# Kernel tuning notes

Hardware: AMD Instinct MI355X
Metric: run time of the kernel (lower is better)

Reference implementation:

```python
import jax, jax.numpy as jnp
import numpy as np
from jax.scipy.special import logsumexp

EPS = 1e-12  # torch F.normalize eps
SINKHORN_ITERS = 3


def _l2norm(a, axis):
    n = jnp.sqrt(jnp.sum(a * a, axis=axis, keepdims=True))
    return a / jnp.maximum(n, EPS)


def _log_optimal_transport(scores, alpha, iters):
    # scores: [B, m, n]; alpha: scalar dust-bin param
    b, m, n = scores.shape
    bins = jnp.broadcast_to(alpha, (b, 1, n)).astype(scores.dtype)
    Z = jnp.concatenate([scores, bins], axis=1)  # [B, m+1, n]
    norm = -np.log(float(m + n))
    log_mu = jnp.asarray(
        np.concatenate([np.full(m, norm), [np.log(float(n - m)) + norm]]),
        scores.dtype,
    )  # [m+1]
    log_nu = jnp.full((n,), norm, scores.dtype)
    u = jnp.zeros((b, m + 1), scores.dtype)
    v = jnp.zeros((b, n), scores.dtype)
    for _ in range(iters):
        u = log_mu[None, :] - logsumexp(Z + v[:, None, :], axis=2)
        v = log_nu[None, :] - logsumexp(Z + u[:, :, None], axis=1)
    return Z + u[:, :, None] + v[:, None, :] - norm


def _forward(x, t, tw1, tb1, tw2, tb2, cw1, cb1, cw2, cb2, sw1, sb1, sw2, sb2, dust_bin):
    B, C = x.shape[0], x.shape[1]
    xf = x.reshape(B, C, -1)  # [B, C, N], 1x1 convs act per-location
    # cluster features f: [B, l, N]
    h = jax.nn.relu(jnp.einsum('oc,bcn->bon', cw1, xf) + cb1[None, :, None])
    f = jnp.einsum('oc,bcn->bon', cw2, h) + cb2[None, :, None]
    # global token: [B, g]
    tok = jax.nn.relu(t @ tw1.T + tb1) @ tw2.T + tb2
    # assignment scores p: [B, m, N]
    hs = jax.nn.relu(jnp.einsum('oc,bcn->bon', sw1, xf) + sb1[None, :, None])
    p = jnp.einsum('oc,bcn->bon', sw2, hs) + sb2[None, :, None]
    Z = _log_optimal_transport(p, dust_bin, SINKHORN_ITERS)
    P = jnp.exp(Z)[:, :-1, :]  # drop dust bin row -> [B, m, N]
    # VLAD-style aggregation: the repeat/multiply/sum is just a batched matmul
    agg = jnp.einsum('bln,bmn->blm', f, P)  # [B, l, m]
    agg = _l2norm(agg, axis=1).reshape(B, -1)  # intra-normalize over l, flatten l-major
    out = jnp.concatenate([_l2norm(tok, axis=-1), agg], axis=-1)
    return _l2norm(out, axis=-1)


def setup_inputs() -> dict:
    key = jax.random.key(0)
    ks = jax.random.split(key, 14)
    B, C, H, W = 64, 768, 32, 32
    L, M, G, HID = 128, 64, 256, 512

    def p(k, shape):
        return jax.random.normal(k, shape, jnp.float32) * 0.02

    return {
        'x': jax.random.normal(ks[0], (B, C, H, W), jnp.float32),
        't': jax.random.normal(ks[1], (B, C), jnp.float32),
        'tw1': p(ks[2], (HID, C)), 'tb1': jnp.zeros((HID,), jnp.float32),
        'tw2': p(ks[3], (G, HID)), 'tb2': jnp.zeros((G,), jnp.float32),
        'cw1': p(ks[4], (HID, C)), 'cb1': jnp.zeros((HID,), jnp.float32),
        'cw2': p(ks[5], (L, HID)), 'cb2': jnp.zeros((L,), jnp.float32),
        'sw1': p(ks[6], (HID, C)), 'sb1': jnp.zeros((HID,), jnp.float32),
        'sw2': p(ks[7], (M, HID)), 'sb2': jnp.zeros((M,), jnp.float32),
        'dust_bin': jnp.asarray(1.0, jnp.float32),
    }


def reference(x, t, tw1, tb1, tw2, tb2, cw1, cb1, cw2, cb2, sw1, sb1, sw2, sb2, dust_bin):
    return _forward(x, t, tw1, tb1, tw2, tb2, cw1, cb1, cw2, cb2, sw1, sb1, sw2, sb2, dust_bin)
```

## Files before the change

### kernel.cpp

```cpp
#include <hip/hip_runtime.h>
#include <math.h>


#define B_SZ   64
#define C_IN   768
#define N_LOC  1024
#define HID    512
#define L_DIM  128
#define M_DIM  64
#define G_DIM  256
#define OUTD   (G_DIM + L_DIM * M_DIM)

typedef unsigned short u16;
typedef __bf16 bf16x8 __attribute__((ext_vector_type(8)));
typedef float f32x4 __attribute__((ext_vector_type(4)));

typedef const __attribute__((address_space(1))) void* gptr_t;
typedef __attribute__((address_space(3))) void* sptr_t;

__device__ __forceinline__ void load_lds16(const void* g, void* l) {
    __builtin_amdgcn_global_load_lds((gptr_t)g, (sptr_t)l, 16, 0, 0);
}

__device__ __forceinline__ u16 f2bf(float f) {
    unsigned u = __float_as_uint(f);
    u += 0x7fffu + ((u >> 16) & 1u);
    return (u16)(u >> 16);
}
__device__ __forceinline__ float bf2f(u16 h) {
    return __uint_as_float(((unsigned)h) << 16);
}

__device__ __forceinline__ float waveReduceSum(float v) {
#pragma unroll
    for (int off = 32; off > 0; off >>= 1) v += __shfl_xor(v, off, 64);
    return v;
}

__global__ __launch_bounds__(256) void setup_kernel(
        const float* __restrict__ cw1, const float* __restrict__ sw1,
        const float* __restrict__ cw2, const float* __restrict__ sw2,
        u16* __restrict__ cw1p, u16* __restrict__ sw1p,
        u16* __restrict__ cw2p, u16* __restrict__ sw2p,
        const float* __restrict__ t, const float* __restrict__ tw1,
        const float* __restrict__ tb1, float* __restrict__ hidb) {
    __shared__ __align__(16) float tl[C_IN];
    const int blk = blockIdx.x;
    const int tid = threadIdx.x;

    if (blk < 432) {
        const int q = blk * 256 + tid;
        const float* src;
        u16* dst;
        if (q < 98304) {
            int path = q / 49152, r = q % 49152;
            int kch = r / 512, c = r & 511;
            src = (path ? sw1 : cw1) + (size_t)c * C_IN + kch * 8;
            dst = (path ? sw1p : cw1p) + (size_t)r * 8;
        } else {
            int q2 = q - 98304;
            int path = (q2 >= 8192) ? 1 : 0;
            int r = q2 - (path ? 8192 : 0);
            int S2 = path ? M_DIM : L_DIM;
            int k2 = r / (4 * S2), kc = (r / S2) & 3, c = r % S2;
            src = (path ? sw2 : cw2) + (size_t)c * HID + k2 * 32 + kc * 8;
            dst = (path ? sw2p : cw2p) + (size_t)r * 8;
        }
        float4 v0 = *(const float4*)(src);
        float4 v1 = *(const float4*)(src + 4);
        *(ushort4*)(dst) = make_ushort4(f2bf(v0.x), f2bf(v0.y), f2bf(v0.z), f2bf(v0.w));
        *(ushort4*)(dst + 4) = make_ushort4(f2bf(v1.x), f2bf(v1.y), f2bf(v1.z), f2bf(v1.w));
        return;
    }

    const int by = blk - 432;
    const int j0 = (by & 7) * 64;
    const int b = by >> 3;
    const int lane = tid & 63;
    const int wave = tid >> 6;
    for (int i = tid; i < C_IN; i += 256) tl[i] = t[(size_t)b * C_IN + i];
    __syncthreads();
    for (int j = wave; j < 64; j += 4) {
        const int row = j0 + j;
        const float4* wr = (const float4*)(tw1 + (size_t)row * C_IN);
        const float4* tr = (const float4*)tl;
        float s = 0.f;
#pragma unroll
        for (int q = 0; q < 3; ++q) {
            float4 wv = wr[lane + 64 * q];
            float4 tv = tr[lane + 64 * q];
            s += wv.x * tv.x + wv.y * tv.y + wv.z * tv.z + wv.w * tv.w;
        }
        s = waveReduceSum(s);
        if (lane == 0) hidb[(size_t)b * HID + row] = fmaxf(s + tb1[row], 0.f);
    }
}

__global__ __launch_bounds__(256, 2) void fused12(
        const float* __restrict__ x,
        const u16* __restrict__ cw1p, const float* __restrict__ cb1,
        const u16* __restrict__ cw2p, const float* __restrict__ cb2,
        const u16* __restrict__ sw1p, const float* __restrict__ sb1,
        const u16* __restrict__ sw2p, const float* __restrict__ sb2,
        u16* __restrict__ fT, u16* __restrict__ pT) {
    __shared__ __align__(16) u16 LDSu[36864];
    const int tid = threadIdx.x;
    const int lane = tid & 63;
    const int wc = tid >> 6;

    const int id = blockIdx.x + 16 * blockIdx.y + 32 * blockIdx.z;
    const int nid = (id & 7) * 256 + (id >> 3);
    const int bx = nid & 15;
    const int path = (nid >> 4) & 1;
    const int bz = nid >> 5;
    const int r0 = bx * 64;

    const u16* W1p = path ? sw1p : cw1p;
    const float* B1 = path ? sb1 : cb1;
    const u16* W2p = path ? sw2p : cw2p;
    const float* B2 = path ? sb2 : cb2;
    u16* O2 = path ? pT : fT;
    const int S2 = path ? M_DIM : L_DIM;

    const float* xb = x + (size_t)bz * C_IN * N_LOC + r0 + (tid & 63) +
                      (size_t)(tid >> 6) * 8 * N_LOC;

    f32x4 acc1[4][8];
#pragma unroll
    for (int mi = 0; mi < 4; ++mi)
#pragma unroll
        for (int ni = 0; ni < 8; ++ni)
            acc1[mi][ni] = (f32x4){0.f, 0.f, 0.f, 0.f};

    const int nk = C_IN / 32;

#define XLOAD(XR_, kt_)                                                        \
    do {                                                                       \
        _Pragma("unroll")                                                      \
        for (int j_ = 0; j_ < 8; ++j_)                                         \
            XR_[j_] = xb[(size_t)((kt_) * 32 + j_) * N_LOC];                   \
    } while (0)

#define AWRITE(db_, XR_)                                                       \
    do {                                                                       \
        uint4 w_;                                                              \
        w_.x = (unsigned)f2bf(XR_[0]) | ((unsigned)f2bf(XR_[1]) << 16);        \
        w_.y = (unsigned)f2bf(XR_[2]) | ((unsigned)f2bf(XR_[3]) << 16);        \
        w_.z = (unsigned)f2bf(XR_[4]) | ((unsigned)f2bf(XR_[5]) << 16);        \
        w_.w = (unsigned)f2bf(XR_[6]) | ((unsigned)f2bf(XR_[7]) << 16);        \
        *(uint4*)(&LDSu[(db_) * 2048 + tid * 8]) = w_;                         \
    } while (0)

#define STG_B(db_, kt_)                                                        \
    do {                                                                       \
        _Pragma("unroll")                                                      \
        for (int j_ = 0; j_ < 8; ++j_)                                         \
            load_lds16(W1p + (size_t)(kt_) * 16384 + (size_t)(j_ * 256 + tid) * 8, \
                       &LDSu[4096 + (db_) * 16384 + (j_ * 256 + tid) * 8]);    \
    } while (0)

#define AV_PTR(db_, mi_)                                                       \
    ((const bf16x8*)&LDSu[(db_) * 2048 + (lane >> 4) * 512 +                   \
                          (16 * (mi_) + (lane & 15)) * 8])
#define BW_PTR(db_, ni_)                                                       \
    ((const bf16x8*)&LDSu[4096 + (db_) * 16384 + (lane >> 4) * 4096 +          \
                          (128 * wc + 16 * (ni_) + (lane & 15)) * 8])

#define TILE_BODY(T_, DB_, XC_, XN_)                                           \
    {                                                                          \
        bf16x8 av[4], bw[8];                                                   \
        _Pragma("unroll")                                                      \
        for (int mi = 0; mi < 4; ++mi) av[mi] = *AV_PTR(DB_, mi);              \
        _Pragma("unroll")                                                      \
        for (int ni = 0; ni < 8; ++ni) bw[ni] = *BW_PTR(DB_, ni);              \
        if ((T_) + 1 < nk) STG_B((DB_) ^ 1, (T_) + 1);                         \
        if ((T_) + 2 < nk) XLOAD(XN_, (T_) + 2);                               \
        asm volatile("s_waitcnt lgkmcnt(0)" ::: "memory");                     \
        __builtin_amdgcn_sched_barrier(0);                                     \
        __builtin_amdgcn_s_barrier();                                          \
        if ((T_) + 1 < nk) AWRITE((DB_) ^ 1, XC_);                             \
        __builtin_amdgcn_s_setprio(1);                                         \
        _Pragma("unroll")                                                      \
        for (int mi = 0; mi < 4; ++mi)                                         \
            _Pragma("unroll")                                                  \
            for (int ni = 0; ni < 8; ++ni)                                     \
                acc1[mi][ni] = __builtin_amdgcn_mfma_f32_16x16x32_bf16(        \
                    av[mi], bw[ni], acc1[mi][ni], 0, 0, 0);                    \
        __builtin_amdgcn_s_setprio(0);                                         \
        __builtin_amdgcn_sched_barrier(0);                                     \
        asm volatile("s_waitcnt lgkmcnt(0)" ::: "memory");                     \
        if ((T_) + 2 < nk)                                                     \
            asm volatile("s_waitcnt vmcnt(8)" ::: "memory");                   \
        else                                                                   \
            asm volatile("s_waitcnt vmcnt(0)" ::: "memory");                   \
        __builtin_amdgcn_s_barrier();                                          \
    }

    float xrA[8], xrB[8];

    STG_B(0, 0);
    XLOAD(xrA, 0);
    AWRITE(0, xrA);
    XLOAD(xrB, 1);
    asm volatile("s_waitcnt lgkmcnt(0)" ::: "memory");
    __builtin_amdgcn_s_barrier();

    for (int tt = 0; tt < nk; tt += 2) {
        TILE_BODY(tt, 0, xrB, xrA);
        TILE_BODY(tt + 1, 1, xrA, xrB);
    }
#undef XLOAD
#undef AWRITE
#undef STG_B
#undef AV_PTR
#undef BW_PTR
#undef TILE_BODY

    {
        float bv1[8];
#pragma unroll
        for (int ni = 0; ni < 8; ++ni)
            bv1[ni] = B1[128 * wc + 16 * ni + (lane & 15)];
#pragma unroll
        for (int mi = 0; mi < 4; ++mi)
#pragma unroll
            for (int ni = 0; ni < 8; ++ni)
#pragma unroll
                for (int rr = 0; rr < 4; ++rr) {
                    int n = 16 * mi + (lane >> 4) * 4 + rr;
                    int c = 128 * wc + 16 * ni + (lane & 15);
                    float v = fmaxf(acc1[mi][ni][rr] + bv1[ni], 0.f);
                    LDSu[(c >> 3) * 512 + n * 8 + (c & 7)] = f2bf(v);
                }
    }
    __syncthreads();

    f32x4 acc2[4][2];
#pragma unroll
    for (int mi = 0; mi < 4; ++mi) {
        acc2[mi][0] = (f32x4){0.f, 0.f, 0.f, 0.f};
        acc2[mi][1] = (f32x4){0.f, 0.f, 0.f, 0.f};
    }
    const int c2base = (S2 == L_DIM) ? 32 * wc : 16 * wc;
    const int cA = c2base + (lane & 15);
    const int cB = c2base + 16 + (lane & 15);
    const int fb0 = (lane >> 4) * S2 + cA;
    const int fb1 = (lane >> 4) * S2 + cB;

    bf16x8 w0n = *(const bf16x8*)(W2p + (size_t)fb0 * 8);
    bf16x8 w1n = {};
    if (S2 == L_DIM) w1n = *(const bf16x8*)(W2p + (size_t)fb1 * 8);

    for (int k2 = 0; k2 < 16; ++k2) {
        bf16x8 w0 = w0n, w1 = w1n;
        if (k2 < 15) {
            w0n = *(const bf16x8*)(W2p + ((size_t)(k2 + 1) * 4 * S2 + fb0) * 8);
            if (S2 == L_DIM)
                w1n = *(const bf16x8*)(W2p + ((size_t)(k2 + 1) * 4 * S2 + fb1) * 8);
        }
        bf16x8 a2[4];
#pragma unroll
        for (int mi = 0; mi < 4; ++mi)
            a2[mi] = *(const bf16x8*)&LDSu[(k2 * 4 + (lane >> 4)) * 512 +
                                           (16 * mi + (lane & 15)) * 8];
#pragma unroll
        for (int mi = 0; mi < 4; ++mi) {
            acc2[mi][0] = __builtin_amdgcn_mfma_f32_16x16x32_bf16(
                a2[mi], w0, acc2[mi][0], 0, 0, 0);
            if (S2 == L_DIM)
                acc2[mi][1] = __builtin_amdgcn_mfma_f32_16x16x32_bf16(
                    a2[mi], w1, acc2[mi][1], 0, 0, 0);
        }
    }

    const float b20 = B2[cA];
    const float b21 = (S2 == L_DIM) ? B2[cB] : 0.f;
    u16* Ob = O2 + (size_t)bz * N_LOC * S2;
#pragma unroll
    for (int mi = 0; mi < 4; ++mi)
#pragma unroll
        for (int rr = 0; rr < 4; ++rr) {
            int row = r0 + 16 * mi + (lane >> 4) * 4 + rr;
            Ob[(size_t)row * S2 + cA] = f2bf(acc2[mi][0][rr] + b20);
            if (S2 == L_DIM)
                Ob[(size_t)row * S2 + cB] = f2bf(acc2[mi][1][rr] + b21);
        }
}

__global__ __launch_bounds__(1024) void sinkhorn_kernel(const u16* __restrict__ pT,
                                                        const float* __restrict__ dust,
                                                        u16* __restrict__ PTb) {
    __shared__ u16 sp[M_DIM][N_LOC];
    __shared__ float eu[M_DIM + 1];
    __shared__ float ev[N_LOC];
    const int b = blockIdx.x;
    const int t = threadIdx.x;
    const int lane = t & 63;
    const int wave = t >> 6;
    const float alpha = dust[0];
    const float Ea = __expf(alpha);
    const float mu = 1.f / 1088.f;
    const float mu64 = 960.f / 1088.f;
    const float nu = 1.f / 1088.f;

    const uint4* prow = (const uint4*)(pT + ((size_t)b * N_LOC + t) * M_DIM);
#pragma unroll
    for (int q = 0; q < 8; ++q) {
        uint4 ch = prow[q];
        sp[q * 8 + 0][t] = (u16)(ch.x);
        sp[q * 8 + 1][t] = (u16)(ch.x >> 16);
        sp[q * 8 + 2][t] = (u16)(ch.y);
        sp[q * 8 + 3][t] = (u16)(ch.y >> 16);
        sp[q * 8 + 4][t] = (u16)(ch.z);
        sp[q * 8 + 5][t] = (u16)(ch.z >> 16);
        sp[q * 8 + 6][t] = (u16)(ch.w);
        sp[q * 8 + 7][t] = (u16)(ch.w >> 16);
    }
#pragma unroll
    for (int m = 0; m < M_DIM; ++m)
        sp[m][t] = f2bf(__expf(bf2f(sp[m][t])));
    ev[t] = 1.f;
    __syncthreads();

    for (int it = 0; it < 3; ++it) {
        for (int m = wave; m < M_DIM + 1; m += 16) {
            float s = 0.f;
            if (m < M_DIM) {
#pragma unroll
                for (int q = 0; q < 16; ++q) {
                    int c = lane + 64 * q;
                    s += bf2f(sp[m][c]) * ev[c];
                }
            } else {
#pragma unroll
                for (int q = 0; q < 16; ++q) {
                    int c = lane + 64 * q;
                    s += ev[c];
                }
                s *= Ea;
            }
            s = waveReduceSum(s);
            if (lane == 0) eu[m] = ((m < M_DIM) ? mu : mu64) / s;
        }
        __syncthreads();
        float s = Ea * eu[M_DIM];
#pragma unroll 8
        for (int m = 0; m < M_DIM; ++m) s += bf2f(sp[m][t]) * eu[m];
        ev[t] = nu / s;
        __syncthreads();
    }

    const float evt = ev[t] * 1088.f;
    u16* Prow = PTb + ((size_t)b * N_LOC + t) * M_DIM;
#pragma unroll
    for (int m8 = 0; m8 < M_DIM; m8 += 8) {
        unsigned v0 = f2bf(bf2f(sp[m8 + 0][t]) * eu[m8 + 0] * evt);
        unsigned v1 = f2bf(bf2f(sp[m8 + 1][t]) * eu[m8 + 1] * evt);
        unsigned v2 = f2bf(bf2f(sp[m8 + 2][t]) * eu[m8 + 2] * evt);
        unsigned v3 = f2bf(bf2f(sp[m8 + 3][t]) * eu[m8 + 3] * evt);
        unsigned v4 = f2bf(bf2f(sp[m8 + 4][t]) * eu[m8 + 4] * evt);
        unsigned v5 = f2bf(bf2f(sp[m8 + 5][t]) * eu[m8 + 5] * evt);
        unsigned v6 = f2bf(bf2f(sp[m8 + 6][t]) * eu[m8 + 6] * evt);
        unsigned v7 = f2bf(bf2f(sp[m8 + 7][t]) * eu[m8 + 7] * evt);
        uint4 w;
        w.x = v0 | (v1 << 16);
        w.y = v2 | (v3 << 16);
        w.z = v4 | (v5 << 16);
        w.w = v6 | (v7 << 16);
        *(uint4*)(Prow + m8) = w;
    }
}

__global__ __launch_bounds__(256) void agg_final_kernel(
        const u16* __restrict__ fT, const u16* __restrict__ PTb,
        const float* __restrict__ hidb, const float* __restrict__ tw2,
        const float* __restrict__ tb2, float* __restrict__ out) {
    __shared__ __align__(16) float SH[9760];
    const int b = blockIdx.y;
    const int bx = blockIdx.x;
    const int tid = threadIdx.x;
    const int lane = tid & 63;
    const int wave = tid >> 6;
    const float EPS = 1e-12f;
    const float rs65 = 1.f / sqrtf(65.f);
    float* ob = out + (size_t)b * OUTD;

    if (bx == 4) {
        float* hl = SH;
        float* tk = SH + 512;
        float* red = SH + 768;
        for (int i = tid; i < HID; i += 256) hl[i] = hidb[(size_t)b * HID + i];
        __syncthreads();
        for (int j = wave; j < G_DIM; j += 4) {
            const float4* wr = (const float4*)(tw2 + (size_t)j * HID);
            const float4* hr = (const float4*)hl;
            float s = 0.f;
#pragma unroll
            for (int q = 0; q < 2; ++q) {
                float4 wv = wr[lane + 64 * q];
                float4 hv = hr[lane + 64 * q];
                s += wv.x * hv.x + wv.y * hv.y + wv.z * hv.z + wv.w * hv.w;
            }
            s = waveReduceSum(s);
            if (lane == 0) tk[j] = s + tb2[j];
        }
        __syncthreads();
        const float tv = tk[tid];
        float ssl = tv * tv;
        ssl = waveReduceSum(ssl);
        if (lane == 0) red[wave] = ssl;
        __syncthreads();
        const float stok = red[0] + red[1] + red[2] + red[3];
        const float rt = rs65 / fmaxf(sqrtf(stok), EPS);
        ob[tid] = tv * rt;
        return;
    }

    const int m0 = bx * 16;
    float* Fs = SH;
    float* Ps = SH + 8448;
    float* ag = SH;
    float* rm = SH + 9728;
    const u16* fb = fT + (size_t)b * N_LOC * L_DIM;
    const u16* Pb = PTb + (size_t)b * N_LOC * M_DIM;

    const int sn = tid >> 2;
    const int fl = (tid & 3) * 32;
    const int pm = (tid & 3) * 4;
    const int tl = (tid >> 3) * 4;
    const int tm = (tid & 7) * 2;

    float acc[4][2] = {};

    for (int n0 = 0; n0 < N_LOC; n0 += 64) {
        __syncthreads();
#pragma unroll
        for (int j = 0; j < 4; ++j) {
            uint4 ld = *(const uint4*)(fb + (size_t)(n0 + sn) * L_DIM + fl + j * 8);
            float4 lo = make_float4(bf2f((u16)(ld.x)), bf2f((u16)(ld.x >> 16)),
                                    bf2f((u16)(ld.y)), bf2f((u16)(ld.y >> 16)));
            float4 hi = make_float4(bf2f((u16)(ld.z)), bf2f((u16)(ld.z >> 16)),
                                    bf2f((u16)(ld.w)), bf2f((u16)(ld.w >> 16)));
            *(float4*)&Fs[sn * 132 + fl + j * 8] = lo;
            *(float4*)&Fs[sn * 132 + fl + j * 8 + 4] = hi;
        }
        {
            uint2 ld = *(const uint2*)(Pb + (size_t)(n0 + sn) * M_DIM + m0 + pm);
            float4 v = make_float4(bf2f((u16)(ld.x)), bf2f((u16)(ld.x >> 16)),
                                   bf2f((u16)(ld.y)), bf2f((u16)(ld.y >> 16)));
            *(float4*)&Ps[sn * 20 + pm] = v;
        }
        __syncthreads();
#pragma unroll 8
        for (int nn = 0; nn < 64; ++nn) {
            float4 a = *(const float4*)&Fs[nn * 132 + tl];
            float p0 = Ps[nn * 20 + tm];
            float p1 = Ps[nn * 20 + tm + 1];
            acc[0][0] = fmaf(a.x, p0, acc[0][0]);
            acc[0][1] = fmaf(a.x, p1, acc[0][1]);
            acc[1][0] = fmaf(a.y, p0, acc[1][0]);
            acc[1][1] = fmaf(a.y, p1, acc[1][1]);
            acc[2][0] = fmaf(a.z, p0, acc[2][0]);
            acc[2][1] = fmaf(a.z, p1, acc[2][1]);
            acc[3][0] = fmaf(a.w, p0, acc[3][0]);
            acc[3][1] = fmaf(a.w, p1, acc[3][1]);
        }
    }

    __syncthreads();
#pragma unroll
    for (int i = 0; i < 4; ++i) {
        ag[(tl + i) * 17 + tm] = acc[i][0];
        ag[(tl + i) * 17 + tm + 1] = acc[i][1];
    }
    __syncthreads();
    if (tid < 16) {
        float ss = 0.f;
#pragma unroll 8
        for (int l = 0; l < L_DIM; ++l) {
            float xv = ag[l * 17 + tid];
            ss = fmaf(xv, xv, ss);
        }
        rm[tid] = rs65 / fmaxf(sqrtf(ss), EPS);
    }
    __syncthreads();
    const float r0 = rm[tm];
    const float r1 = rm[tm + 1];
#pragma unroll
    for (int i = 0; i < 4; ++i) {
        ob[G_DIM + (tl + i) * M_DIM + m0 + tm] = acc[i][0] * r0;
        ob[G_DIM + (tl + i) * M_DIM + m0 + tm + 1] = acc[i][1] * r1;
    }
}

extern "C" void kernel_launch(void* const* d_in, const int* in_sizes, int n_in,
                              void* d_out, int out_size, void* d_ws, size_t ws_size,
                              hipStream_t stream) {
    const float* x    = (const float*)d_in[0];
    const float* t    = (const float*)d_in[1];
    const float* tw1  = (const float*)d_in[2];
    const float* tb1  = (const float*)d_in[3];
    const float* tw2  = (const float*)d_in[4];
    const float* tb2  = (const float*)d_in[5];
    const float* cw1  = (const float*)d_in[6];
    const float* cb1  = (const float*)d_in[7];
    const float* cw2  = (const float*)d_in[8];
    const float* cb2  = (const float*)d_in[9];
    const float* sw1  = (const float*)d_in[10];
    const float* sb1  = (const float*)d_in[11];
    const float* sw2  = (const float*)d_in[12];
    const float* sb2  = (const float*)d_in[13];
    const float* dust = (const float*)d_in[14];
    float* out = (float*)d_out;

    char* ws = (char*)d_ws;
    u16* fT    = (u16*)(ws + 100663296ull);
    u16* pT    = (u16*)(ws + 117440512ull);
    u16* cw1p  = (u16*)(ws + 125829120ull);
    u16* sw1p  = (u16*)(ws + 126615552ull);
    u16* cw2p  = (u16*)(ws + 127401984ull);
    u16* sw2p  = (u16*)(ws + 127533056ull);
    float* hidb = (float*)(ws + 127598592ull);
    u16* PTb   = (u16*)(ws);

    setup_kernel<<<944, 256, 0, stream>>>(cw1, sw1, cw2, sw2,
                                          cw1p, sw1p, cw2p, sw2p,
                                          t, tw1, tb1, hidb);

    fused12<<<dim3(16, 2, B_SZ), 256, 0, stream>>>(
        x, cw1p, cb1, cw2p, cb2, sw1p, sb1, sw2p, sb2, fT, pT);

    sinkhorn_kernel<<<B_SZ, 1024, 0, stream>>>(pT, dust, PTb);
    agg_final_kernel<<<dim3(5, B_SZ), 256, 0, stream>>>(fT, PTb, hidb, tw2, tb2, out);
}
```

Before: 253.4 us.

## Split fused conv hidden dimension into two passes to raise occupancy

```diff
diff --git a/kernel.cpp b/kernel.cpp
--- a/kernel.cpp
+++ b/kernel.cpp
@@ -96,14 +96,14 @@
     }
 }
 
-__global__ __launch_bounds__(256, 2) void fused12(
+__global__ __launch_bounds__(256, 3) void fused12(
         const float* __restrict__ x,
         const u16* __restrict__ cw1p, const float* __restrict__ cb1,
         const u16* __restrict__ cw2p, const float* __restrict__ cb2,
         const u16* __restrict__ sw1p, const float* __restrict__ sb1,
         const u16* __restrict__ sw2p, const float* __restrict__ sb2,
         u16* __restrict__ fT, u16* __restrict__ pT) {
-    __shared__ __align__(16) u16 LDSu[36864];
+    __shared__ __align__(16) u16 LDSu[20480];
     const int tid = threadIdx.x;
     const int lane = tid & 63;
     const int wc = tid >> 6;
@@ -125,14 +125,19 @@
     const float* xb = x + (size_t)bz * C_IN * N_LOC + r0 + (tid & 63) +
                       (size_t)(tid >> 6) * 8 * N_LOC;
 
-    f32x4 acc1[4][8];
-#pragma unroll
-    for (int mi = 0; mi < 4; ++mi)
-#pragma unroll
-        for (int ni = 0; ni < 8; ++ni)
-            acc1[mi][ni] = (f32x4){0.f, 0.f, 0.f, 0.f};
-
     const int nk = C_IN / 32;
+
+    f32x4 acc2[4][2];
+#pragma unroll
+    for (int mi = 0; mi < 4; ++mi) {
+        acc2[mi][0] = (f32x4){0.f, 0.f, 0.f, 0.f};
+        acc2[mi][1] = (f32x4){0.f, 0.f, 0.f, 0.f};
+    }
+    const int c2base = (S2 == L_DIM) ? 32 * wc : 16 * wc;
+    const int cA = c2base + (lane & 15);
+    const int cB = c2base + 16 + (lane & 15);
+    const int fb0 = (lane >> 4) * S2 + cA;
+    const int fb1 = (lane >> 4) * S2 + cB;
 
 #define XLOAD(XR_, kt_)                                                        \
     do {                                                                       \
@@ -154,41 +159,39 @@
 #define STG_B(db_, kt_)                                                        \
     do {                                                                       \
         _Pragma("unroll")                                                      \
-        for (int j_ = 0; j_ < 8; ++j_)                                         \
-            load_lds16(W1p + (size_t)(kt_) * 16384 + (size_t)(j_ * 256 + tid) * 8, \
-                       &LDSu[4096 + (db_) * 16384 + (j_ * 256 + tid) * 8]);    \
+        for (int j_ = 0; j_ < 4; ++j_)                                         \
+            load_lds16(W1p + ((size_t)((kt_) * 4 + j_) * 512 + 256 * pass + tid) * 8, \
+                       &LDSu[4096 + (db_) * 8192 + (j_ * 256 + tid) * 8]);     \
     } while (0)
 
 #define AV_PTR(db_, mi_)                                                       \
     ((const bf16x8*)&LDSu[(db_) * 2048 + (lane >> 4) * 512 +                   \
                           (16 * (mi_) + (lane & 15)) * 8])
 #define BW_PTR(db_, ni_)                                                       \
-    ((const bf16x8*)&LDSu[4096 + (db_) * 16384 + (lane >> 4) * 4096 +          \
-                          (128 * wc + 16 * (ni_) + (lane & 15)) * 8])
+    ((const bf16x8*)&LDSu[4096 + (db_) * 8192 + (lane >> 4) * 2048 +           \
+                          (64 * wc + 16 * (ni_) + (lane & 15)) * 8])
 
 #define TILE_BODY(T_, DB_, XC_, XN_)                                           \
     {                                                                          \
-        bf16x8 av[4], bw[8];                                                   \
+        const int db_ = (DB_);                                                 \
+        bf16x8 av[4], bw[4];                                                   \
         _Pragma("unroll")                                                      \
-        for (int mi = 0; mi < 4; ++mi) av[mi] = *AV_PTR(DB_, mi);              \
+        for (int mi = 0; mi < 4; ++mi) av[mi] = *AV_PTR(db_, mi);              \
         _Pragma("unroll")                                                      \
-        for (int ni = 0; ni < 8; ++ni) bw[ni] = *BW_PTR(DB_, ni);              \
-        if ((T_) + 1 < nk) STG_B((DB_) ^ 1, (T_) + 1);                         \
+        for (int ni = 0; ni < 4; ++ni) bw[ni] = *BW_PTR(db_, ni);              \
+        if ((T_) + 1 < nk) STG_B(db_ ^ 1, (T_) + 1);                           \
         if ((T_) + 2 < nk) XLOAD(XN_, (T_) + 2);                               \
-        asm volatile("s_waitcnt lgkmcnt(0)" ::: "memory");                     \
-        __builtin_amdgcn_sched_barrier(0);                                     \
-        __builtin_amdgcn_s_barrier();                                          \
-        if ((T_) + 1 < nk) AWRITE((DB_) ^ 1, XC_);                             \
         __builtin_amdgcn_s_setprio(1);                                         \
         _Pragma("unroll")                                                      \
         for (int mi = 0; mi < 4; ++mi)                                         \
             _Pragma("unroll")                                                  \
-            for (int ni = 0; ni < 8; ++ni)                                     \
+            for (int ni = 0; ni < 4; ++ni)                                     \
                 acc1[mi][ni] = __builtin_amdgcn_mfma_f32_16x16x32_bf16(        \
                     av[mi], bw[ni], acc1[mi][ni], 0, 0, 0);                    \
         __builtin_amdgcn_s_setprio(0);                                         \
+        if ((T_) + 1 < nk) AWRITE(db_ ^ 1, XC_);                               \
+        asm volatile("s_waitcnt lgkmcnt(0)" ::: "memory");                     \
         __builtin_amdgcn_sched_barrier(0);                                     \
-        asm volatile("s_waitcnt lgkmcnt(0)" ::: "memory");                     \
         if ((T_) + 2 < nk)                                                     \
             asm volatile("s_waitcnt vmcnt(8)" ::: "memory");                   \
         else                                                                   \
@@ -198,16 +201,74 @@
 
     float xrA[8], xrB[8];
 
-    STG_B(0, 0);
-    XLOAD(xrA, 0);
-    AWRITE(0, xrA);
-    XLOAD(xrB, 1);
-    asm volatile("s_waitcnt lgkmcnt(0)" ::: "memory");
-    __builtin_amdgcn_s_barrier();
-
-    for (int tt = 0; tt < nk; tt += 2) {
-        TILE_BODY(tt, 0, xrB, xrA);
-        TILE_BODY(tt + 1, 1, xrA, xrB);
+    for (int pass = 0; pass < 2; ++pass) {
+        f32x4 acc1[4][4];
+#pragma unroll
+        for (int mi = 0; mi < 4; ++mi)
+#pragma unroll
+            for (int ni = 0; ni < 4; ++ni)
+                acc1[mi][ni] = (f32x4){0.f, 0.f, 0.f, 0.f};
+
+        STG_B(0, 0);
+        XLOAD(xrA, 0);
+        AWRITE(0, xrA);
+        XLOAD(xrB, 1);
+        asm volatile("s_waitcnt lgkmcnt(0)" ::: "memory");
+        __builtin_amdgcn_s_barrier();
+
+        for (int tt = 0; tt < nk; tt += 2) {
+            TILE_BODY(tt + 0, 0, xrB, xrA);
+            TILE_BODY(tt + 1, 1, xrA, xrB);
+        }
+
+        {
+            float bv1[4];
+#pragma unroll
+            for (int ni = 0; ni < 4; ++ni)
+                bv1[ni] = B1[256 * pass + 64 * wc + 16 * ni + (lane & 15)];
+#pragma unroll
+            for (int mi = 0; mi < 4; ++mi)
+#pragma unroll
+                for (int ni = 0; ni < 4; ++ni)
+#pragma unroll
+                    for (int rr = 0; rr < 4; ++rr) {
+                        int n = 16 * mi + (lane >> 4) * 4 + rr;
+                        int cl = 64 * wc + 16 * ni + (lane & 15);
+                        float v = fmaxf(acc1[mi][ni][rr] + bv1[ni], 0.f);
+                        LDSu[4096 + (cl >> 3) * 512 + n * 8 + (cl & 7)] = f2bf(v);
+                    }
+        }
+        __syncthreads();
+
+        {
+            bf16x8 w0n = *(const bf16x8*)(W2p + ((size_t)(8 * pass) * 4 * S2 + fb0) * 8);
+            bf16x8 w1n = {};
+            if (S2 == L_DIM)
+                w1n = *(const bf16x8*)(W2p + ((size_t)(8 * pass) * 4 * S2 + fb1) * 8);
+            for (int k2l = 0; k2l < 8; ++k2l) {
+                bf16x8 w0 = w0n, w1 = w1n;
+                if (k2l < 7) {
+                    const size_t kb = (size_t)(8 * pass + k2l + 1) * 4 * S2;
+                    w0n = *(const bf16x8*)(W2p + (kb + fb0) * 8);
+                    if (S2 == L_DIM)
+                        w1n = *(const bf16x8*)(W2p + (kb + fb1) * 8);
+                }
+                bf16x8 a2[4];
+#pragma unroll
+                for (int mi = 0; mi < 4; ++mi)
+                    a2[mi] = *(const bf16x8*)&LDSu[4096 +
+                        (k2l * 4 + (lane >> 4)) * 512 + (16 * mi + (lane & 15)) * 8];
+#pragma unroll
+                for (int mi = 0; mi < 4; ++mi) {
+                    acc2[mi][0] = __builtin_amdgcn_mfma_f32_16x16x32_bf16(
+                        a2[mi], w0, acc2[mi][0], 0, 0, 0);
+                    if (S2 == L_DIM)
+                        acc2[mi][1] = __builtin_amdgcn_mfma_f32_16x16x32_bf16(
+                            a2[mi], w1, acc2[mi][1], 0, 0, 0);
+                }
+            }
+        }
+        __syncthreads();
     }
 #undef XLOAD
 #undef AWRITE
@@ -215,63 +276,6 @@
 #undef AV_PTR
 #undef BW_PTR
 #undef TILE_BODY
-
-    {
-        float bv1[8];
-#pragma unroll
-        for (int ni = 0; ni < 8; ++ni)
-            bv1[ni] = B1[128 * wc + 16 * ni + (lane & 15)];
-#pragma unroll
-        for (int mi = 0; mi < 4; ++mi)
-#pragma unroll
-            for (int ni = 0; ni < 8; ++ni)
-#pragma unroll
-                for (int rr = 0; rr < 4; ++rr) {
-                    int n = 16 * mi + (lane >> 4) * 4 + rr;
-                    int c = 128 * wc + 16 * ni + (lane & 15);
-                    float v = fmaxf(acc1[mi][ni][rr] + bv1[ni], 0.f);
-                    LDSu[(c >> 3) * 512 + n * 8 + (c & 7)] = f2bf(v);
-                }
-    }
-    __syncthreads();
-
-    f32x4 acc2[4][2];
-#pragma unroll
-    for (int mi = 0; mi < 4; ++mi) {
-        acc2[mi][0] = (f32x4){0.f, 0.f, 0.f, 0.f};
-        acc2[mi][1] = (f32x4){0.f, 0.f, 0.f, 0.f};
-    }
-    const int c2base = (S2 == L_DIM) ? 32 * wc : 16 * wc;
-    const int cA = c2base + (lane & 15);
-    const int cB = c2base + 16 + (lane & 15);
-    const int fb0 = (lane >> 4) * S2 + cA;
-    const int fb1 = (lane >> 4) * S2 + cB;
-
-    bf16x8 w0n = *(const bf16x8*)(W2p + (size_t)fb0 * 8);
-    bf16x8 w1n = {};
-    if (S2 == L_DIM) w1n = *(const bf16x8*)(W2p + (size_t)fb1 * 8);
-
-    for (int k2 = 0; k2 < 16; ++k2) {
-        bf16x8 w0 = w0n, w1 = w1n;
-        if (k2 < 15) {
-            w0n = *(const bf16x8*)(W2p + ((size_t)(k2 + 1) * 4 * S2 + fb0) * 8);
-            if (S2 == L_DIM)
-                w1n = *(const bf16x8*)(W2p + ((size_t)(k2 + 1) * 4 * S2 + fb1) * 8);
-        }
-        bf16x8 a2[4];
-#pragma unroll
-        for (int mi = 0; mi < 4; ++mi)
-            a2[mi] = *(const bf16x8*)&LDSu[(k2 * 4 + (lane >> 4)) * 512 +
-                                           (16 * mi + (lane & 15)) * 8];
-#pragma unroll
-        for (int mi = 0; mi < 4; ++mi) {
-            acc2[mi][0] = __builtin_amdgcn_mfma_f32_16x16x32_bf16(
-                a2[mi], w0, acc2[mi][0], 0, 0, 0);
-            if (S2 == L_DIM)
-                acc2[mi][1] = __builtin_amdgcn_mfma_f32_16x16x32_bf16(
-                    a2[mi], w1, acc2[mi][1], 0, 0, 0);
-        }
-    }
 
     const float b20 = B2[cA];
     const float b21 = (S2 == L_DIM) ? B2[cB] : 0.f;
```

Result: slower. 286.6 us (+13.1%).
